# Performance work log

Measured on AMD Instinct MI355X. Metric: run time of the kernel, lower is better.

## Reference

```python
import jax, jax.numpy as jnp
import numpy as np

D_MODEL = 1024
NUM_HEADS = 16
WINDOW = 128
DEPTH = D_MODEL // NUM_HEADS


def setup_inputs() -> dict:
    key = jax.random.key(0)
    ks = jax.random.split(key, 9)
    B, S = 2, 2048
    scale = 1.0 / np.sqrt(D_MODEL)
    x = jax.random.normal(ks[0], (B, S, D_MODEL), dtype=jnp.float32)
    Wq = jax.random.normal(ks[1], (D_MODEL, D_MODEL), dtype=jnp.float32) * scale
    Wk = jax.random.normal(ks[2], (D_MODEL, D_MODEL), dtype=jnp.float32) * scale
    Wv = jax.random.normal(ks[3], (D_MODEL, D_MODEL), dtype=jnp.float32) * scale
    Wo = jax.random.normal(ks[4], (D_MODEL, D_MODEL), dtype=jnp.float32) * scale
    bq = jnp.zeros((D_MODEL,), jnp.float32)
    bk = jnp.zeros((D_MODEL,), jnp.float32)
    bv = jnp.zeros((D_MODEL,), jnp.float32)
    bo = jnp.zeros((D_MODEL,), jnp.float32)
    return {"x": x, "Wq": Wq, "bq": bq, "Wk": Wk, "bk": bk,
            "Wv": Wv, "bv": bv, "Wo": Wo, "bo": bo}


def _split_heads(t, B, S):
    # [B,S,D] -> [B,H,S,depth]
    return t.reshape(B, S, NUM_HEADS, DEPTH).transpose(0, 2, 1, 3)


def reference(x, Wq, bq, Wk, bk, Wv, bv, Wo, bo):
    B, S, _ = x.shape
    q = _split_heads(x @ Wq + bq, B, S)
    k = _split_heads(x @ Wk + bk, B, S)
    v = _split_heads(x @ Wv + bv, B, S)
    scores = jnp.einsum('bhqd,bhkd->bhqk', q, k) / jnp.sqrt(jnp.float32(DEPTH))
    idx = jnp.arange(S)
    # mask[i_row=j, i_col=i] per original: |i - j| <= window (symmetric)
    local = jnp.abs(idx[None, :] - idx[:, None]) <= WINDOW  # [S,S]
    scores = jnp.where(local[None, None], scores, jnp.float32(-1e9))
    attn = jax.nn.softmax(scores, axis=-1)
    out = jnp.einsum('bhqk,bhkd->bhqd', attn, v)
    concat = out.transpose(0, 2, 1, 3).reshape(B, S, D_MODEL)
    return concat @ Wo + bo
```

## Files before the change

kernel.cpp:

```cpp
#include <hip/hip_runtime.h>
#include <cstdint>
#include <cstddef>

typedef __attribute__((ext_vector_type(8))) short short8;
typedef __attribute__((ext_vector_type(4))) short short4v;
typedef __attribute__((ext_vector_type(4))) float f32x4;
typedef short8 bf16x8;

typedef __attribute__((address_space(1))) const unsigned GU;
typedef __attribute__((address_space(3))) unsigned LU;

__device__ __forceinline__ short f2bf(float f) {
  unsigned u = __builtin_bit_cast(unsigned, f);
  u += 0x7fffu + ((u >> 16) & 1u);
  return (short)(u >> 16);
}

__global__ __launch_bounds__(256) void k_prep(const float* __restrict__ x,
                                              const float* __restrict__ W0, const float* __restrict__ W1,
                                              const float* __restrict__ W2, const float* __restrict__ W3,
                                              short* __restrict__ xb, short* __restrict__ WT) {
  __shared__ short T[64 * 72];
  int bid = blockIdx.x;
  int tid = threadIdx.x;
  if (bid < 2048) {
    size_t i = ((size_t)bid * 256 + tid) * 8;
    f32x4 a = *(const f32x4*)(x + i);
    f32x4 b = *(const f32x4*)(x + i + 4);
    short8 o;
#pragma unroll
    for (int j = 0; j < 4; ++j) { o[j] = f2bf(a[j]); o[4 + j] = f2bf(b[j]); }
    *(short8*)(xb + i) = o;
    return;
  }
  bid -= 2048;
  int widx = bid >> 8;
  int t = bid & 255;
  int kr = (t >> 4) * 64, nc = (t & 15) * 64;
  const float* W = widx == 0 ? W0 : widx == 1 ? W1 : widx == 2 ? W2 : W3;
  short* out = WT + (size_t)widx * 1048576;
#pragma unroll
  for (int i = 0; i < 4; ++i) {
    int idx = tid + i * 256;
    int k = idx >> 4, n4 = (idx & 15) << 2;
    f32x4 v = *(const f32x4*)(W + (size_t)(kr + k) * 1024 + nc + n4);
#pragma unroll
    for (int j = 0; j < 4; ++j) T[(n4 + j) * 72 + k] = f2bf(v[j]);
  }
  __syncthreads();
#pragma unroll
  for (int i = 0; i < 2; ++i) {
    int idx = tid + i * 256;
    int n = idx >> 3, k8 = (idx & 7) << 3;
    *(short8*)(out + (size_t)(nc + n) * 1024 + kr + k8) = *(const short8*)&T[n * 72 + k8];
  }
}

__global__ __launch_bounds__(512, 1) void k_gemm256(
    const short* __restrict__ A, const short* __restrict__ BT,
    const float* __restrict__ bias0, const float* __restrict__ bias1, const float* __restrict__ bias2,
    short* __restrict__ outb) {
  __shared__ short S[57344];
  const int tid = threadIdx.x;
  const int lane = tid & 63, w = tid >> 6;
  const int g = lane >> 4, qi = lane & 15;
  const int wm = w >> 2, wn = w & 3;
  int bid = blockIdx.x;
  int xcd = bid & 7, ii = bid >> 3;
  const int tm = (xcd >> 1) * 4 + (ii >> 3);
  const int tn = (xcd & 1) * 8 + (ii & 7);
  const int m0 = tm * 256, n0 = tn * 192;
  const size_t K = 1024;
  const short* Ab = A + (size_t)m0 * K;
  const short* Bb = BT + (size_t)n0 * K;

  auto stage64 = [&](int roff, const short* gbase, int kt) {
    int r = tid >> 3;
    int js = ((tid & 7) ^ (r & 7)) << 3;
    __builtin_amdgcn_global_load_lds((GU*)(gbase + (size_t)r * K + kt * 64 + js),
                                     (LU*)(&S[roff + tid * 8]), 16, 0, 0);
  };
  auto lda_a = [&](int bbase, int mf, int kk) -> bf16x8 {
    int row = (mf & 3) * 16 + qi;
    int reg = wm * 2 + (mf >> 2);
    return *(const bf16x8*)&S[bbase + reg * 4096 + row * 64 + (((kk * 4 + g) ^ (row & 7)) << 3)];
  };
  auto lda_b = [&](int bbase, int nf, int kk) -> bf16x8 {
    int c = wn * 48 + nf * 16 + qi;
    int reg = c >> 6, row = c & 63;
    return *(const bf16x8*)&S[bbase + 16384 + reg * 4096 + row * 64 + (((kk * 4 + g) ^ (row & 7)) << 3)];
  };

  f32x4 acc[8][3];
#pragma unroll
  for (int i = 0; i < 8; ++i)
#pragma unroll
    for (int j = 0; j < 3; ++j) acc[i][j] = (f32x4)(0.0f);

#define MFA(mi, ni, av, bv) \
  acc[mi][ni] = __builtin_amdgcn_mfma_f32_16x16x32_bf16(av, bv, acc[mi][ni], 0, 0, 0)
#define MF12(Aa, Bb_, o) \
  MFA((o)+0,0,(Aa)[(o)+0],(Bb_)[0]); MFA((o)+0,1,(Aa)[(o)+0],(Bb_)[1]); MFA((o)+0,2,(Aa)[(o)+0],(Bb_)[2]); \
  MFA((o)+1,0,(Aa)[(o)+1],(Bb_)[0]); MFA((o)+1,1,(Aa)[(o)+1],(Bb_)[1]); MFA((o)+1,2,(Aa)[(o)+1],(Bb_)[2]); \
  MFA((o)+2,0,(Aa)[(o)+2],(Bb_)[0]); MFA((o)+2,1,(Aa)[(o)+2],(Bb_)[1]); MFA((o)+2,2,(Aa)[(o)+2],(Bb_)[2]); \
  MFA((o)+3,0,(Aa)[(o)+3],(Bb_)[0]); MFA((o)+3,1,(Aa)[(o)+3],(Bb_)[1]); MFA((o)+3,2,(Aa)[(o)+3],(Bb_)[2])
#define SB __builtin_amdgcn_sched_barrier(0)
#define PHASE_TAIL(MFMAS) do { \
    SB; \
    __builtin_amdgcn_s_barrier(); \
    asm volatile("s_waitcnt lgkmcnt(0)" ::: "memory"); \
    SB; \
    __builtin_amdgcn_s_setprio(1); \
    MFMAS; \
    __builtin_amdgcn_s_setprio(0); \
    SB; \
    __builtin_amdgcn_s_barrier(); \
  } while (0)

  stage64(0,     Ab,            0);
  stage64(4096,  Ab + 65536,    0);
  stage64(8192,  Ab + 131072,   0);
  stage64(12288, Ab + 196608,   0);
  stage64(16384, Bb,            0);
  stage64(20480, Bb + 65536,    0);
  stage64(24576, Bb + 131072,   0);
  stage64(28672 + 16384, Bb,          1);
  stage64(28672 + 20480, Bb + 65536,  1);
  stage64(28672 + 24576, Bb + 131072, 1);
  asm volatile("s_waitcnt vmcnt(3)" ::: "memory");
  __builtin_amdgcn_s_barrier();

  for (int t = 0; t < 16; ++t) {
    const int b = t & 1, nb = b ^ 1;
    const int bb = b * 28672, nbb = nb * 28672;
    const int t1 = t + 1 < 15 ? t + 1 : 15;
    const int t2 = t + 2 < 15 ? t + 2 : 15;
    bf16x8 aA[8], aB[3], cA[8], cB[3];

#pragma unroll
    for (int mf = 0; mf < 4; ++mf) aA[mf] = lda_a(bb, mf, 0);
#pragma unroll
    for (int nf = 0; nf < 3; ++nf) aB[nf] = lda_b(bb, nf, 0);
    stage64(nbb,        Ab,         t1);
    stage64(nbb + 4096, Ab + 65536, t1);
    PHASE_TAIL(MF12(aA, aB, 0));
#pragma unroll
    for (int mf = 4; mf < 8; ++mf) aA[mf] = lda_a(bb, mf, 0);
#pragma unroll
    for (int nf = 0; nf < 3; ++nf) cB[nf] = lda_b(bb, nf, 1);
    stage64(nbb + 8192,  Ab + 131072, t1);
    stage64(nbb + 12288, Ab + 196608, t1);
    PHASE_TAIL(MF12(aA, aB, 4));
#pragma unroll
    for (int mf = 0; mf < 4; ++mf) cA[mf] = lda_a(bb, mf, 1);
    stage64(bb + 16384, Bb,         t2);
    stage64(bb + 20480, Bb + 65536, t2);
    PHASE_TAIL(MF12(cA, cB, 0));
#pragma unroll
    for (int mf = 4; mf < 8; ++mf) cA[mf] = lda_a(bb, mf, 1);
    stage64(bb + 24576, Bb + 131072, t2);
    asm volatile("s_waitcnt vmcnt(3)" ::: "memory");
    PHASE_TAIL(MF12(cA, cB, 4));
  }
#undef PHASE_TAIL
#undef MF12
#undef MFA
#undef SB

  asm volatile("s_waitcnt vmcnt(0)" ::: "memory");
  __syncthreads();
  float bv[3];
#pragma unroll
  for (int nf = 0; nf < 3; ++nf) {
    int colg = n0 + wn * 48 + nf * 16 + qi;
    int sel = colg >> 10;
    const float* bias = sel == 0 ? bias0 : (sel == 1 ? bias1 : bias2);
    bv[nf] = bias[colg & 1023];
  }
  short* Ep = S;
#pragma unroll
  for (int p = 0; p < 2; ++p) {
    __syncthreads();
    if (wm == p) {
#pragma unroll
      for (int mf = 0; mf < 8; ++mf)
#pragma unroll
        for (int nf = 0; nf < 3; ++nf)
#pragma unroll
          for (int j = 0; j < 4; ++j)
            Ep[(mf * 16 + g * 4 + j) * 200 + wn * 48 + nf * 16 + qi] =
                f2bf(acc[mf][nf][j] + bv[nf]);
    }
    __syncthreads();
#pragma unroll
    for (int i = 0; i < 6; ++i) {
      int idx = tid + i * 512;
      int r = idx / 24, c8 = (idx % 24) * 8;
      int grow = m0 + p * 128 + r;
      int colg = n0 + c8;
      int sel = colg >> 10;
      *(short8*)&outb[(size_t)sel * 4194304 + (size_t)grow * 1024 + (colg & 1023)] =
          *(const short8*)&Ep[r * 200 + c8];
    }
  }
}

__global__ __launch_bounds__(256, 2) void k_gemmO(
    const short* __restrict__ A, const short* __restrict__ BT,
    const float* __restrict__ bias0, float* __restrict__ outf) {
  __shared__ short Smem[16384];
  const int tid = threadIdx.x;
  const int lane = tid & 63, w = tid >> 6;
  const int g = lane >> 4, qi = lane & 15;
  const int wr = (w >> 1) * 64, wc = (w & 1) * 64;
  const int m0 = blockIdx.y * 128, n0 = blockIdx.x * 128;
  const size_t K = 1024;
  const short* Ab = A + (size_t)m0 * K;
  const short* Bb = BT + (size_t)n0 * K;

  auto stage = [&](int buf, int k0) {
    short* Asb = Smem + buf * 4096;
    short* Bsb = Smem + 8192 + buf * 4096;
#pragma unroll
    for (int i = 0; i < 2; ++i) {
      int cidx = tid + i * 256;
      int r = cidx >> 2;
      int csw = ((cidx & 3) ^ ((r >> 1) & 3)) << 3;
      __builtin_amdgcn_global_load_lds((GU*)(Ab + (size_t)r * K + k0 + csw),
                                       (LU*)(&Asb[cidx * 8]), 16, 0, 0);
      __builtin_amdgcn_global_load_lds((GU*)(Bb + (size_t)r * K + k0 + csw),
                                       (LU*)(&Bsb[cidx * 8]), 16, 0, 0);
    }
  };

  f32x4 acc[4][4];
#pragma unroll
  for (int i = 0; i < 4; ++i)
#pragma unroll
    for (int j = 0; j < 4; ++j) acc[i][j] = (f32x4)(0.0f);

  stage(0, 0);
  __syncthreads();
  for (int kt = 0; kt < 32; ++kt) {
    int cur = kt & 1;
    if (kt < 31) stage(cur ^ 1, (kt + 1) * 32);
    const short* Asb = Smem + cur * 4096;
    const short* Bsb = Smem + 8192 + cur * 4096;
    bf16x8 a[4], b[4];
#pragma unroll
    for (int mf = 0; mf < 4; ++mf) {
      int R = wr + mf * 16 + qi;
      a[mf] = *(const bf16x8*)&Asb[R * 32 + ((g ^ ((R >> 1) & 3)) << 3)];
    }
#pragma unroll
    for (int nf = 0; nf < 4; ++nf) {
      int R = wc + nf * 16 + qi;
      b[nf] = *(const bf16x8*)&Bsb[R * 32 + ((g ^ ((R >> 1) & 3)) << 3)];
    }
#pragma unroll
    for (int mf = 0; mf < 4; ++mf)
#pragma unroll
      for (int nf = 0; nf < 4; ++nf)
        acc[mf][nf] = __builtin_amdgcn_mfma_f32_16x16x32_bf16(a[mf], b[nf], acc[mf][nf], 0, 0, 0);
    __syncthreads();
  }

  float* Ft = (float*)Smem;
  float bv[4];
#pragma unroll
  for (int nf = 0; nf < 4; ++nf) bv[nf] = bias0[n0 + wc + nf * 16 + qi];
#pragma unroll
  for (int mf = 0; mf < 4; ++mf) {
    __syncthreads();
#pragma unroll
    for (int nf = 0; nf < 4; ++nf)
#pragma unroll
      for (int j = 0; j < 4; ++j)
        Ft[((w >> 1) * 16 + g * 4 + j) * 136 + wc + nf * 16 + qi] = acc[mf][nf][j] + bv[nf];
    __syncthreads();
#pragma unroll
    for (int i = 0; i < 4; ++i) {
      int idx = tid + i * 256;
      int r = idx >> 5, c4 = (idx & 31) << 2;
      int row = m0 + ((r >> 4) << 6) + mf * 16 + (r & 15);
      *(f32x4*)&outf[(size_t)row * 1024 + n0 + c4] = *(const f32x4*)&Ft[r * 136 + c4];
    }
  }
}

__global__ __launch_bounds__(256, 2) void k_attn(const short* __restrict__ qg_,
                                                 const short* __restrict__ kg_,
                                                 const short* __restrict__ vg_,
                                                 short* __restrict__ outp) {
  __shared__ short Qs[64 * 72];
  __shared__ short Ks[64 * 72];
  __shared__ short Vs[64 * 72];
  __shared__ short Ps[4][16 * 72];
  int bid = blockIdx.x;
  int qt = bid & 31, h = (bid >> 5) & 15, b = bid >> 9;
  int q0 = qt * 64;
  int tid = threadIdx.x, lane = tid & 63, w = tid >> 6;
  int g = lane >> 4, qi = lane & 15;

  const short* qsrc = qg_ + ((size_t)b * 2048 + q0) * 1024 + h * 64;
#pragma unroll
  for (int i = 0; i < 2; ++i) {
    int idx = tid + i * 256;
    int r = idx >> 3, c = (idx & 7) << 3;
    *(short8*)&Qs[r * 72 + c] = *(const short8*)&qsrc[(size_t)r * 1024 + c];
  }

  float m = -1e30f, l = 0.f;
  f32x4 oacc[4];
#pragma unroll
  for (int i = 0; i < 4; ++i) oacc[i] = (f32x4)(0.0f);
  int qglob = q0 + w * 16 + qi;

  for (int cc = 0; cc < 5; ++cc) {
    int kb0 = q0 - 128 + cc * 64;
    if (kb0 < 0 || kb0 >= 2048) continue;
    __syncthreads();
    const short* ksrc = kg_ + ((size_t)b * 2048 + kb0) * 1024 + h * 64;
    const short* vsrc = vg_ + ((size_t)b * 2048 + kb0) * 1024 + h * 64;
#pragma unroll
    for (int i = 0; i < 2; ++i) {
      int idx = tid + i * 256;
      int r = idx >> 3, c = (idx & 7) << 3;
      *(short8*)&Ks[r * 72 + c] = *(const short8*)&ksrc[(size_t)r * 1024 + c];
      short8 vv = *(const short8*)&vsrc[(size_t)r * 1024 + c];
#pragma unroll
      for (int j = 0; j < 8; ++j) {
        int d = c + j;
        Vs[d * 72 + ((r + ((d >> 3) << 3)) & 63)] = vv[j];
      }
    }
    __syncthreads();

    f32x4 st[4];
#pragma unroll
    for (int i = 0; i < 4; ++i) st[i] = (f32x4)(0.0f);
#pragma unroll
    for (int ds = 0; ds < 2; ++ds) {
      bf16x8 qf = *(const bf16x8*)&Qs[(w * 16 + qi) * 72 + ds * 32 + g * 8];
#pragma unroll
      for (int mf = 0; mf < 4; ++mf) {
        bf16x8 kf = *(const bf16x8*)&Ks[(mf * 16 + qi) * 72 + ds * 32 + g * 8];
        st[mf] = __builtin_amdgcn_mfma_f32_16x16x32_bf16(kf, qf, st[mf], 0, 0, 0);
      }
    }

    float pv[16];
    float pm = -1e30f;
#pragma unroll
    for (int mf = 0; mf < 4; ++mf)
#pragma unroll
      for (int j = 0; j < 4; ++j) {
        int kcol = kb0 + mf * 16 + g * 4 + j;
        float s = st[mf][j] * 0.125f;
        int d = kcol - qglob;
        bool valid = (d >= -128) && (d <= 128);
        s = valid ? s : -1e30f;
        pv[mf * 4 + j] = s;
        pm = fmaxf(pm, s);
      }
    pm = fmaxf(pm, __shfl_xor(pm, 16));
    pm = fmaxf(pm, __shfl_xor(pm, 32));
    float mnew = fmaxf(m, pm);
    float scale = __expf(m - mnew);
    float ls = 0.f;
#pragma unroll
    for (int e = 0; e < 16; ++e) {
      float p = pv[e] > -1e29f ? __expf(pv[e] - mnew) : 0.f;
      pv[e] = p;
      ls += p;
    }
    ls += __shfl_xor(ls, 16);
    ls += __shfl_xor(ls, 32);
    l = l * scale + ls;
    m = mnew;
#pragma unroll
    for (int mf = 0; mf < 4; ++mf) oacc[mf] *= scale;

#pragma unroll
    for (int f = 0; f < 4; ++f) {
      short4v pk;
#pragma unroll
      for (int j = 0; j < 4; ++j) pk[j] = f2bf(pv[f * 4 + j]);
      *(short4v*)&Ps[w][qi * 72 + f * 16 + g * 4] = pk;
    }

#pragma unroll
    for (int ks = 0; ks < 2; ++ks) {
      bf16x8 pf = *(const bf16x8*)&Ps[w][qi * 72 + ks * 32 + g * 8];
#pragma unroll
      for (int mf = 0; mf < 4; ++mf) {
        int dd = mf * 16 + qi;
        int pc = ((ks * 32 + g * 8) + ((dd >> 3) << 3)) & 63;
        bf16x8 vf = *(const bf16x8*)&Vs[dd * 72 + pc];
        oacc[mf] = __builtin_amdgcn_mfma_f32_16x16x32_bf16(vf, pf, oacc[mf], 0, 0, 0);
      }
    }
  }

  __syncthreads();
  short* Os = Ks;
  float inv = 1.f / l;
#pragma unroll
  for (int mf = 0; mf < 4; ++mf) {
    short4v pk;
#pragma unroll
    for (int j = 0; j < 4; ++j) pk[j] = f2bf(oacc[mf][j] * inv);
    *(short4v*)&Os[(w * 16 + qi) * 72 + mf * 16 + g * 4] = pk;
  }
  __syncthreads();
  short* dst = outp + ((size_t)b * 2048 + q0) * 1024 + h * 64;
  int r = tid >> 2, c16 = (tid & 3) << 4;
  *(short8*)&dst[(size_t)r * 1024 + c16] = *(const short8*)&Os[r * 72 + c16];
  *(short8*)&dst[(size_t)r * 1024 + c16 + 8] = *(const short8*)&Os[r * 72 + c16 + 8];
}

extern "C" void kernel_launch(void* const* d_in, const int* in_sizes, int n_in,
                              void* d_out, int out_size, void* d_ws, size_t ws_size,
                              hipStream_t stream) {
  const float* x  = (const float*)d_in[0];
  const float* Wq = (const float*)d_in[1];
  const float* bq = (const float*)d_in[2];
  const float* Wk = (const float*)d_in[3];
  const float* bk = (const float*)d_in[4];
  const float* Wv = (const float*)d_in[5];
  const float* bv = (const float*)d_in[6];
  const float* Wo = (const float*)d_in[7];
  const float* bo = (const float*)d_in[8];

  short* ws = (short*)d_ws;
  short* xb       = ws;
  short* qkv      = ws + 4194304;
  short* vbuf     = qkv + 2 * 4194304;
  short* attn_out = ws;
  short* WT       = ws + 4 * 4194304;

  k_prep<<<3072, 256, 0, stream>>>(x, Wq, Wk, Wv, Wo, xb, WT);
  k_gemm256<<<256, 512, 0, stream>>>(xb, WT, bq, bk, bv, qkv);
  k_attn<<<1024, 256, 0, stream>>>(qkv, qkv + 4194304, vbuf, attn_out);
  {
    dim3 grid(8, 32);
    k_gemmO<<<grid, 256, 0, stream>>>(attn_out, WT + 3 * 1048576, bo, (float*)d_out);
  }
}
```

Measured before the change: 82.20 us.

## Prefetch next K/V tile into registers during attention compute

```diff
diff --git a/kernel.cpp b/kernel.cpp
--- a/kernel.cpp
+++ b/kernel.cpp
@@ -303,12 +303,42 @@
   int g = lane >> 4, qi = lane & 15;
 
   const short* qsrc = qg_ + ((size_t)b * 2048 + q0) * 1024 + h * 64;
+  const short* kbase = kg_ + ((size_t)b * 2048) * 1024 + h * 64;
+  const short* vbase = vg_ + ((size_t)b * 2048) * 1024 + h * 64;
+
+  int sr[2], sc[2];
 #pragma unroll
   for (int i = 0; i < 2; ++i) {
     int idx = tid + i * 256;
-    int r = idx >> 3, c = (idx & 7) << 3;
-    *(short8*)&Qs[r * 72 + c] = *(const short8*)&qsrc[(size_t)r * 1024 + c];
-  }
+    sr[i] = idx >> 3;
+    sc[i] = (idx & 7) << 3;
+  }
+
+  int qk = q0 >> 6;
+  int c_lo = qk < 2 ? 2 - qk : 0;
+  int c_hi = 33 - qk; if (c_hi > 4) c_hi = 4;
+
+#pragma unroll
+  for (int i = 0; i < 2; ++i)
+    *(short8*)&Qs[sr[i] * 72 + sc[i]] = *(const short8*)&qsrc[(size_t)sr[i] * 1024 + sc[i]];
+  {
+    int kb0 = q0 - 128 + c_lo * 64;
+#pragma unroll
+    for (int i = 0; i < 2; ++i) {
+      short8 kv = *(const short8*)&kbase[(size_t)(kb0 + sr[i]) * 1024 + sc[i]];
+      short8 vv = *(const short8*)&vbase[(size_t)(kb0 + sr[i]) * 1024 + sc[i]];
+      *(short8*)&Ks[sr[i] * 72 + sc[i]] = kv;
+#pragma unroll
+      for (int j = 0; j < 8; ++j) {
+        int d = sc[i] + j;
+        Vs[d * 72 + ((sr[i] + ((d >> 3) << 3)) & 63)] = vv[j];
+      }
+    }
+  }
+  __syncthreads();
+
+  bf16x8 qf0 = *(const bf16x8*)&Qs[(w * 16 + qi) * 72 + g * 8];
+  bf16x8 qf1 = *(const bf16x8*)&Qs[(w * 16 + qi) * 72 + 32 + g * 8];
 
   float m = -1e30f, l = 0.f;
   f32x4 oacc[4];
@@ -316,37 +346,28 @@
   for (int i = 0; i < 4; ++i) oacc[i] = (f32x4)(0.0f);
   int qglob = q0 + w * 16 + qi;
 
-  for (int cc = 0; cc < 5; ++cc) {
+  for (int cc = c_lo; cc <= c_hi; ++cc) {
     int kb0 = q0 - 128 + cc * 64;
-    if (kb0 < 0 || kb0 >= 2048) continue;
-    __syncthreads();
-    const short* ksrc = kg_ + ((size_t)b * 2048 + kb0) * 1024 + h * 64;
-    const short* vsrc = vg_ + ((size_t)b * 2048 + kb0) * 1024 + h * 64;
-#pragma unroll
-    for (int i = 0; i < 2; ++i) {
-      int idx = tid + i * 256;
-      int r = idx >> 3, c = (idx & 7) << 3;
-      *(short8*)&Ks[r * 72 + c] = *(const short8*)&ksrc[(size_t)r * 1024 + c];
-      short8 vv = *(const short8*)&vsrc[(size_t)r * 1024 + c];
-#pragma unroll
-      for (int j = 0; j < 8; ++j) {
-        int d = c + j;
-        Vs[d * 72 + ((r + ((d >> 3) << 3)) & 63)] = vv[j];
+    bool pf = cc < c_hi;
+    short8 krn[2], vrn[2];
+    if (pf) {
+      int kb1 = kb0 + 64;
+#pragma unroll
+      for (int i = 0; i < 2; ++i) {
+        krn[i] = *(const short8*)&kbase[(size_t)(kb1 + sr[i]) * 1024 + sc[i]];
+        vrn[i] = *(const short8*)&vbase[(size_t)(kb1 + sr[i]) * 1024 + sc[i]];
       }
     }
-    __syncthreads();
 
     f32x4 st[4];
 #pragma unroll
     for (int i = 0; i < 4; ++i) st[i] = (f32x4)(0.0f);
 #pragma unroll
-    for (int ds = 0; ds < 2; ++ds) {
-      bf16x8 qf = *(const bf16x8*)&Qs[(w * 16 + qi) * 72 + ds * 32 + g * 8];
-#pragma unroll
-      for (int mf = 0; mf < 4; ++mf) {
-        bf16x8 kf = *(const bf16x8*)&Ks[(mf * 16 + qi) * 72 + ds * 32 + g * 8];
-        st[mf] = __builtin_amdgcn_mfma_f32_16x16x32_bf16(kf, qf, st[mf], 0, 0, 0);
-      }
+    for (int mf = 0; mf < 4; ++mf) {
+      bf16x8 kf0 = *(const bf16x8*)&Ks[(mf * 16 + qi) * 72 + g * 8];
+      bf16x8 kf1 = *(const bf16x8*)&Ks[(mf * 16 + qi) * 72 + 32 + g * 8];
+      st[mf] = __builtin_amdgcn_mfma_f32_16x16x32_bf16(kf0, qf0, st[mf], 0, 0, 0);
+      st[mf] = __builtin_amdgcn_mfma_f32_16x16x32_bf16(kf1, qf1, st[mf], 0, 0, 0);
     }
 
     float pv[16];
@@ -391,18 +412,31 @@
 
 #pragma unroll
     for (int ks = 0; ks < 2; ++ks) {
-      bf16x8 pf = *(const bf16x8*)&Ps[w][qi * 72 + ks * 32 + g * 8];
+      bf16x8 pf_ = *(const bf16x8*)&Ps[w][qi * 72 + ks * 32 + g * 8];
 #pragma unroll
       for (int mf = 0; mf < 4; ++mf) {
         int dd = mf * 16 + qi;
         int pc = ((ks * 32 + g * 8) + ((dd >> 3) << 3)) & 63;
         bf16x8 vf = *(const bf16x8*)&Vs[dd * 72 + pc];
-        oacc[mf] = __builtin_amdgcn_mfma_f32_16x16x32_bf16(vf, pf, oacc[mf], 0, 0, 0);
+        oacc[mf] = __builtin_amdgcn_mfma_f32_16x16x32_bf16(vf, pf_, oacc[mf], 0, 0, 0);
       }
     }
-  }
-
-  __syncthreads();
+
+    __syncthreads();
+    if (pf) {
+#pragma unroll
+      for (int i = 0; i < 2; ++i) {
+        *(short8*)&Ks[sr[i] * 72 + sc[i]] = krn[i];
+#pragma unroll
+        for (int j = 0; j < 8; ++j) {
+          int d = sc[i] + j;
+          Vs[d * 72 + ((sr[i] + ((d >> 3) << 3)) & 63)] = vrn[i][j];
+        }
+      }
+    }
+    __syncthreads();
+  }
+
   short* Os = Ks;
   float inv = 1.f / l;
 #pragma unroll
```

Measured after the change: 84.12 us. 1.02x slower.

## Fuse fp32-to-bf16 conversion of x into the QKV GEMM A-tile staging

Applied to the files above, without the earlier changes.

```diff
diff --git a/kernel.cpp b/kernel.cpp
--- a/kernel.cpp
+++ b/kernel.cpp
@@ -16,24 +16,12 @@
   return (short)(u >> 16);
 }
 
-__global__ __launch_bounds__(256) void k_prep(const float* __restrict__ x,
-                                              const float* __restrict__ W0, const float* __restrict__ W1,
+__global__ __launch_bounds__(256) void k_prep(const float* __restrict__ W0, const float* __restrict__ W1,
                                               const float* __restrict__ W2, const float* __restrict__ W3,
-                                              short* __restrict__ xb, short* __restrict__ WT) {
+                                              short* __restrict__ WT) {
   __shared__ short T[64 * 72];
   int bid = blockIdx.x;
   int tid = threadIdx.x;
-  if (bid < 2048) {
-    size_t i = ((size_t)bid * 256 + tid) * 8;
-    f32x4 a = *(const f32x4*)(x + i);
-    f32x4 b = *(const f32x4*)(x + i + 4);
-    short8 o;
-#pragma unroll
-    for (int j = 0; j < 4; ++j) { o[j] = f2bf(a[j]); o[4 + j] = f2bf(b[j]); }
-    *(short8*)(xb + i) = o;
-    return;
-  }
-  bid -= 2048;
   int widx = bid >> 8;
   int t = bid & 255;
   int kr = (t >> 4) * 64, nc = (t & 15) * 64;
@@ -57,7 +45,7 @@
 }
 
 __global__ __launch_bounds__(512, 1) void k_gemm256(
-    const short* __restrict__ A, const short* __restrict__ BT,
+    const float* __restrict__ X, const short* __restrict__ BT,
     const float* __restrict__ bias0, const float* __restrict__ bias1, const float* __restrict__ bias2,
     short* __restrict__ outb) {
   __shared__ short S[57344];
@@ -71,14 +59,25 @@
   const int tn = (xcd & 1) * 8 + (ii & 7);
   const int m0 = tm * 256, n0 = tn * 192;
   const size_t K = 1024;
-  const short* Ab = A + (size_t)m0 * K;
   const short* Bb = BT + (size_t)n0 * K;
 
+  const int sr_ = tid >> 3;
+  const int sj_ = ((tid & 7) ^ (sr_ & 7)) << 3;
+
   auto stage64 = [&](int roff, const short* gbase, int kt) {
-    int r = tid >> 3;
-    int js = ((tid & 7) ^ (r & 7)) << 3;
-    __builtin_amdgcn_global_load_lds((GU*)(gbase + (size_t)r * K + kt * 64 + js),
+    __builtin_amdgcn_global_load_lds((GU*)(gbase + (size_t)sr_ * K + kt * 64 + sj_),
                                      (LU*)(&S[roff + tid * 8]), 16, 0, 0);
+  };
+  auto aloadf = [&](f32x4* dst, int reg, int kt) {
+    const float* src = X + (size_t)(m0 + reg * 64 + sr_) * 1024 + kt * 64 + sj_;
+    dst[0] = *(const f32x4*)src;
+    dst[1] = *(const f32x4*)(src + 4);
+  };
+  auto awrite = [&](const f32x4* src, int roff) {
+    short8 o;
+#pragma unroll
+    for (int j = 0; j < 4; ++j) { o[j] = f2bf(src[0][j]); o[4 + j] = f2bf(src[1][j]); }
+    *(short8*)&S[roff + tid * 8] = o;
   };
   auto lda_a = [&](int bbase, int mf, int kk) -> bf16x8 {
     int row = (mf & 3) * 16 + qi;
@@ -117,18 +116,20 @@
     __builtin_amdgcn_s_barrier(); \
   } while (0)
 
-  stage64(0,     Ab,            0);
-  stage64(4096,  Ab + 65536,    0);
-  stage64(8192,  Ab + 131072,   0);
-  stage64(12288, Ab + 196608,   0);
-  stage64(16384, Bb,            0);
-  stage64(20480, Bb + 65536,    0);
-  stage64(24576, Bb + 131072,   0);
-  stage64(28672 + 16384, Bb,          1);
-  stage64(28672 + 20480, Bb + 65536,  1);
-  stage64(28672 + 24576, Bb + 131072, 1);
-  asm volatile("s_waitcnt vmcnt(3)" ::: "memory");
-  __builtin_amdgcn_s_barrier();
+  {
+    f32x4 p0[2], p1[2], p2[2], p3[2];
+    aloadf(p0, 0, 0); aloadf(p1, 1, 0); aloadf(p2, 2, 0); aloadf(p3, 3, 0);
+    stage64(16384, Bb,            0);
+    stage64(20480, Bb + 65536,    0);
+    stage64(24576, Bb + 131072,   0);
+    stage64(28672 + 16384, Bb,          1);
+    stage64(28672 + 20480, Bb + 65536,  1);
+    stage64(28672 + 24576, Bb + 131072, 1);
+    awrite(p0, 0); awrite(p1, 4096); awrite(p2, 8192); awrite(p3, 12288);
+    asm volatile("s_waitcnt lgkmcnt(0)" ::: "memory");
+    asm volatile("s_waitcnt vmcnt(3)" ::: "memory");
+    __builtin_amdgcn_s_barrier();
+  }
 
   for (int t = 0; t < 16; ++t) {
     const int b = t & 1, nb = b ^ 1;
@@ -136,25 +137,30 @@
     const int t1 = t + 1 < 15 ? t + 1 : 15;
     const int t2 = t + 2 < 15 ? t + 2 : 15;
     bf16x8 aA[8], aB[3], cA[8], cB[3];
-
+    f32x4 fa0[2], fa1[2], fa2[2], fa3[2];
+
+    aloadf(fa0, 0, t1);
+    aloadf(fa1, 1, t1);
 #pragma unroll
     for (int mf = 0; mf < 4; ++mf) aA[mf] = lda_a(bb, mf, 0);
 #pragma unroll
     for (int nf = 0; nf < 3; ++nf) aB[nf] = lda_b(bb, nf, 0);
-    stage64(nbb,        Ab,         t1);
-    stage64(nbb + 4096, Ab + 65536, t1);
     PHASE_TAIL(MF12(aA, aB, 0));
+    aloadf(fa2, 2, t1);
+    aloadf(fa3, 3, t1);
 #pragma unroll
     for (int mf = 4; mf < 8; ++mf) aA[mf] = lda_a(bb, mf, 0);
 #pragma unroll
     for (int nf = 0; nf < 3; ++nf) cB[nf] = lda_b(bb, nf, 1);
-    stage64(nbb + 8192,  Ab + 131072, t1);
-    stage64(nbb + 12288, Ab + 196608, t1);
     PHASE_TAIL(MF12(aA, aB, 4));
-#pragma unroll
-    for (int mf = 0; mf < 4; ++mf) cA[mf] = lda_a(bb, mf, 1);
+    awrite(fa0, nbb);
+    awrite(fa1, nbb + 4096);
+    awrite(fa2, nbb + 8192);
+    awrite(fa3, nbb + 12288);
     stage64(bb + 16384, Bb,         t2);
     stage64(bb + 20480, Bb + 65536, t2);
+#pragma unroll
+    for (int mf = 0; mf < 4; ++mf) cA[mf] = lda_a(bb, mf, 1);
     PHASE_TAIL(MF12(cA, cB, 0));
 #pragma unroll
     for (int mf = 4; mf < 8; ++mf) cA[mf] = lda_a(bb, mf, 1);
@@ -433,14 +439,13 @@
   const float* bo = (const float*)d_in[8];
 
   short* ws = (short*)d_ws;
-  short* xb       = ws;
   short* qkv      = ws + 4194304;
   short* vbuf     = qkv + 2 * 4194304;
   short* attn_out = ws;
   short* WT       = ws + 4 * 4194304;
 
-  k_prep<<<3072, 256, 0, stream>>>(x, Wq, Wk, Wv, Wo, xb, WT);
-  k_gemm256<<<256, 512, 0, stream>>>(xb, WT, bq, bk, bv, qkv);
+  k_prep<<<1024, 256, 0, stream>>>(Wq, Wk, Wv, Wo, WT);
+  k_gemm256<<<256, 512, 0, stream>>>(x, WT, bq, bk, bv, qkv);
   k_attn<<<1024, 256, 0, stream>>>(qkv, qkv + 4194304, vbuf, attn_out);
   {
     dim3 grid(8, 32);
```

Result: slower. 88.20 us (+7.3%).
